# Optimization experiments

Hardware: AMD Instinct MI355X
Metric: run time of the kernel (lower is better)

## Reference

```python
import jax, jax.numpy as jnp
import numpy as np

N_NODES = 50000
N_EDGES = 1_600_000
IN_CH = 128
HID = 128


def setup_inputs() -> dict:
    key = jax.random.key(0)
    ks = jax.random.split(key, 8)
    x = jax.random.normal(ks[0], (N_NODES, IN_CH), dtype=jnp.float32)
    edge_index = jax.random.randint(ks[1], (2, N_EDGES), 0, N_NODES, dtype=jnp.int64)
    def glorot(k, shape):
        fan_in, fan_out = shape
        s = jnp.sqrt(6.0 / (fan_in + fan_out))
        return jax.random.uniform(k, shape, jnp.float32, -s, s)
    return {
        "x": x,
        "edge_index": edge_index,
        "W1": glorot(ks[2], (IN_CH, HID)), "b1": jnp.zeros((HID,), jnp.float32),
        "W2": glorot(ks[3], (HID, HID)), "b2": jnp.zeros((HID,), jnp.float32),
        "W_age": glorot(ks[4], (HID, 3)), "b_age": jnp.zeros((3,), jnp.float32),
        "W_sex": glorot(ks[5], (HID, 2)), "b_sex": jnp.zeros((2,), jnp.float32),
        "W_eth": glorot(ks[6], (HID, 3)), "b_eth": jnp.zeros((3,), jnp.float32),
    }


def _prep_graph(edge_index, n_nodes):
    # PyG GCNConv default: add self-loops, symmetric normalization.
    loops = jnp.arange(n_nodes, dtype=edge_index.dtype)
    src = jnp.concatenate([edge_index[0], loops])
    dst = jnp.concatenate([edge_index[1], loops])
    deg = jax.ops.segment_sum(jnp.ones_like(dst, jnp.float32), dst, num_segments=n_nodes)
    dinv = jnp.where(deg > 0, jax.lax.rsqrt(deg), 0.0)
    norm = dinv[src] * dinv[dst]  # [E+N]
    return src, dst, norm


def _gcn_conv(x, W, b, src, dst, norm, n_nodes):
    h = x @ W                              # [N, out] linear transform first
    msg = h[src] * norm[:, None]           # gather + normalize
    out = jax.ops.segment_sum(msg, dst, num_segments=n_nodes)  # scatter-add
    return out + b


def reference(x, edge_index, W1, b1, W2, b2, W_age, b_age, W_sex, b_sex, W_eth, b_eth):
    n = x.shape[0]
    src, dst, norm = _prep_graph(edge_index, n)
    h = jax.nn.relu(_gcn_conv(x, W1, b1, src, dst, norm, n))
    h = jax.nn.relu(_gcn_conv(h, W2, b2, src, dst, norm, n))
    age = _gcn_conv(h, W_age, b_age, src, dst, norm, n)
    sex = _gcn_conv(h, W_sex, b_sex, src, dst, norm, n)
    eth = _gcn_conv(h, W_eth, b_eth, src, dst, norm, n)
    return age, sex, eth
```

## Files before the change

### kernel.cpp

```cpp
#include <hip/hip_runtime.h>
#include <hip/hip_fp16.h>


#define NBUK_MAX 512

__global__ __launch_bounds__(256) void k_bhist(const int* __restrict__ dst, int E, int nbuk,
                                               int* __restrict__ bcount) {
    __shared__ int h[NBUK_MAX];
    int tid = threadIdx.x;
    for (int i = tid; i < nbuk; i += 256) h[i] = 0;
    __syncthreads();
    int s0 = blockIdx.x * 4096;
#pragma unroll
    for (int i = 0; i < 16; i++) {
        int e = s0 + i * 256 + tid;
        if (e < E) atomicAdd(&h[dst[e] >> 7], 1);
    }
    __syncthreads();
    for (int i = tid; i < nbuk; i += 256)
        if (h[i]) atomicAdd(&bcount[i], h[i]);
}

__global__ __launch_bounds__(512) void k_bscan(const int* __restrict__ bcount, int nb,
                                               int* __restrict__ bbase, int* __restrict__ bcur) {
    __shared__ int s[512];
    int tid = threadIdx.x;
    int v = (tid < nb) ? bcount[tid] : 0;
    s[tid] = v;
    __syncthreads();
    for (int off = 1; off < 512; off <<= 1) {
        int t = (tid >= off) ? s[tid - off] : 0;
        __syncthreads();
        s[tid] += t;
        __syncthreads();
    }
    if (tid < nb) {
        int excl = s[tid] - v;
        bbase[tid] = excl;
        bcur[tid] = excl;
        if (tid == nb - 1) bbase[nb] = s[tid];
    }
}

__global__ __launch_bounds__(256) void k_passA(const int* __restrict__ src,
                                               const int* __restrict__ dst, int E, int nbuk,
                                               int* __restrict__ bcur,
                                               unsigned* __restrict__ bbuf) {
    __shared__ int h[NBUK_MAX];
    __shared__ int base[NBUK_MAX];
    __shared__ int lcur[NBUK_MAX];
    int tid = threadIdx.x;
    for (int i = tid; i < nbuk; i += 256) h[i] = 0;
    __syncthreads();
    int s0 = blockIdx.x * 4096;
#pragma unroll
    for (int i = 0; i < 16; i++) {
        int e = s0 + i * 256 + tid;
        if (e < E) atomicAdd(&h[dst[e] >> 7], 1);
    }
    __syncthreads();
    for (int i = tid; i < nbuk; i += 256) {
        int c = h[i];
        base[i] = c ? atomicAdd(&bcur[i], c) : 0;
        lcur[i] = 0;
    }
    __syncthreads();
#pragma unroll
    for (int i = 0; i < 16; i++) {
        int e = s0 + i * 256 + tid;
        if (e < E) {
            int d = dst[e];
            int b = d >> 7;
            int idx = atomicAdd(&lcur[b], 1);
            bbuf[base[b] + idx] = ((unsigned)d << 16) | (unsigned)src[e];
        }
    }
}

__global__ __launch_bounds__(256) void k_passB(const unsigned* __restrict__ bbuf,
                                               const int* __restrict__ bbase, int N,
                                               int* __restrict__ row_ptr,
                                               float* __restrict__ dinv,
                                               unsigned short* __restrict__ sorted) {
    __shared__ int h[128], sc[128], lc[128];
    int b = blockIdx.x, tid = threadIdx.x;
    int node0 = b << 7;
    int ncnt = min(128, N - node0);
    int s = bbase[b], e = bbase[b + 1];
    if (tid < 128) h[tid] = 0;
    __syncthreads();
    for (int i = s + tid; i < e; i += 256) atomicAdd(&h[(bbuf[i] >> 16) & 127], 1);
    __syncthreads();
    if (tid < 128) sc[tid] = h[tid];
    __syncthreads();
    for (int off = 1; off < 128; off <<= 1) {
        int t = 0;
        if (tid < 128 && tid >= off) t = sc[tid - off];
        __syncthreads();
        if (tid < 128) sc[tid] += t;
        __syncthreads();
    }
    if (tid < ncnt) {
        int excl = sc[tid] - h[tid];
        row_ptr[node0 + tid] = s + excl;
        dinv[node0 + tid] = rsqrtf((float)(h[tid] + 1));
        lc[tid] = excl;
    }
    if (b == gridDim.x - 1 && tid == 0) row_ptr[N] = e;
    __syncthreads();
    for (int i = s + tid; i < e; i += 256) {
        unsigned p = bbuf[i];
        int nl = (p >> 16) & 127;
        int idx = atomicAdd(&lc[nl], 1);
        sorted[s + idx] = (unsigned short)(p & 0xffffu);
    }
}

__global__ __launch_bounds__(256) void k_gemm_scale_h(const float* __restrict__ in,
                                                      const float* __restrict__ W,
                                                      const float* __restrict__ dinv, int N,
                                                      __half* __restrict__ out) {
    __shared__ float Ws[32][128];
    __shared__ float Xs[32][64];
    int tid = threadIdx.x;
    int row0 = blockIdx.x * 64;
    int tc = tid & 15;
    int tr = tid >> 4;
    float acc[4][8];
#pragma unroll
    for (int i = 0; i < 4; i++)
#pragma unroll
        for (int j = 0; j < 8; j++) acc[i][j] = 0.f;

    for (int k0 = 0; k0 < 128; k0 += 32) {
#pragma unroll
        for (int j = 0; j < 4; j++) {
            int u = tid + j * 256;
            int kk = u >> 5, c4 = u & 31;
            *(float4*)&Ws[kk][c4 * 4] = *(const float4*)&W[(k0 + kk) * 128 + c4 * 4];
        }
#pragma unroll
        for (int j = 0; j < 2; j++) {
            int u = tid + j * 256;
            int r = u >> 3, kq = u & 7;
            int row = row0 + r;
            if (row > N - 1) row = N - 1;
            float4 v = *(const float4*)&in[(size_t)row * 128 + k0 + kq * 4];
            Xs[kq * 4 + 0][r] = v.x;
            Xs[kq * 4 + 1][r] = v.y;
            Xs[kq * 4 + 2][r] = v.z;
            Xs[kq * 4 + 3][r] = v.w;
        }
        __syncthreads();
#pragma unroll 8
        for (int kk = 0; kk < 32; kk++) {
            float4 xv = *(const float4*)&Xs[kk][tr * 4];
            float4 wa = *(const float4*)&Ws[kk][tc * 8];
            float4 wb = *(const float4*)&Ws[kk][tc * 8 + 4];
            float xr[4] = {xv.x, xv.y, xv.z, xv.w};
            float wc[8] = {wa.x, wa.y, wa.z, wa.w, wb.x, wb.y, wb.z, wb.w};
#pragma unroll
            for (int i = 0; i < 4; i++)
#pragma unroll
                for (int j = 0; j < 8; j++) acc[i][j] += xr[i] * wc[j];
        }
        __syncthreads();
    }
#pragma unroll
    for (int i = 0; i < 4; i++) {
        int row = row0 + tr * 4 + i;
        if (row < N) {
            float di = dinv[row];
            union {
                uint4 u;
                __half h[8];
            } pk;
#pragma unroll
            for (int j = 0; j < 8; j++) pk.h[j] = __float2half_rn(di * acc[i][j]);
            *(uint4*)&out[(size_t)row * 128 + tc * 8] = pk.u;
        }
    }
}

__global__ __launch_bounds__(256) void k_agg128h(const __half* __restrict__ hs,
                                                 const int* __restrict__ row_ptr,
                                                 const unsigned short* __restrict__ ss,
                                                 const float* __restrict__ dinv,
                                                 const float* __restrict__ bias, int N,
                                                 int do_relu, float* __restrict__ out) {
    int wid = threadIdx.x >> 6;
    int lane = threadIdx.x & 63;
    int node = blockIdx.x * 4 + wid;
    if (node >= N) return;
    const __half2* hp = (const __half2*)hs;
    float2 acc = __half22float2(hp[(size_t)node * 64 + lane]);
    int s = row_ptr[node], e = row_ptr[node + 1];
    int i = s;
    for (; i + 4 <= e; i += 4) {
        int s0 = ss[i], s1 = ss[i + 1], s2 = ss[i + 2], s3 = ss[i + 3];
        float2 v0 = __half22float2(hp[(size_t)s0 * 64 + lane]);
        float2 v1 = __half22float2(hp[(size_t)s1 * 64 + lane]);
        float2 v2 = __half22float2(hp[(size_t)s2 * 64 + lane]);
        float2 v3 = __half22float2(hp[(size_t)s3 * 64 + lane]);
        acc.x += (v0.x + v1.x) + (v2.x + v3.x);
        acc.y += (v0.y + v1.y) + (v2.y + v3.y);
    }
    for (; i < e; i++) {
        float2 v0 = __half22float2(hp[(size_t)ss[i] * 64 + lane]);
        acc.x += v0.x;
        acc.y += v0.y;
    }
    float di = dinv[node];
    int c = lane * 2;
    float2 b = *(const float2*)&bias[c];
    float ox = di * acc.x + b.x;
    float oy = di * acc.y + b.y;
    if (do_relu) {
        ox = fmaxf(ox, 0.f);
        oy = fmaxf(oy, 0.f);
    }
    *(float2*)&out[(size_t)node * 128 + c] = {ox, oy};
}

__global__ __launch_bounds__(256) void k_headgemm(const float* __restrict__ h,
                                                  const float* __restrict__ Wa,
                                                  const float* __restrict__ Wsx,
                                                  const float* __restrict__ We,
                                                  const float* __restrict__ dinv, int N,
                                                  float* __restrict__ ths) {
    __shared__ float Ws8[128][8];
    int tid = threadIdx.x;
#pragma unroll
    for (int j = 0; j < 4; j++) {
        int u = tid + j * 256;
        int k = u >> 3, c = u & 7;
        float v;
        if (c < 3) v = Wa[k * 3 + c];
        else if (c < 5) v = Wsx[k * 2 + (c - 3)];
        else v = We[k * 3 + (c - 5)];
        Ws8[k][c] = v;
    }
    __syncthreads();
    int node = blockIdx.x * 32 + (tid >> 3);
    int col = tid & 7;
    if (node >= N) return;
    const float* hr = &h[(size_t)node * 128];
    float acc = 0.f;
#pragma unroll 4
    for (int k = 0; k < 128; k += 4) {
        float4 hv = *(const float4*)&hr[k];
        acc += hv.x * Ws8[k][col] + hv.y * Ws8[k + 1][col] + hv.z * Ws8[k + 2][col] +
               hv.w * Ws8[k + 3][col];
    }
    ths[(size_t)node * 8 + col] = dinv[node] * acc;
}

__global__ __launch_bounds__(256) void k_agg8(const float* __restrict__ ths,
                                              const int* __restrict__ row_ptr,
                                              const unsigned short* __restrict__ ss,
                                              const float* __restrict__ dinv,
                                              const float* __restrict__ ba,
                                              const float* __restrict__ bs,
                                              const float* __restrict__ be, int N,
                                              float* __restrict__ outp) {
    int tid = threadIdx.x;
    int node = blockIdx.x * 32 + (tid >> 3);
    int j = tid & 7;
    if (node >= N) return;
    float acc = ths[(size_t)node * 8 + j];
    int s = row_ptr[node], e = row_ptr[node + 1];
    for (int i = s; i < e; i++) {
        int sc = ss[i];
        acc += ths[(size_t)sc * 8 + j];
    }
    float bias = (j < 3) ? ba[j] : ((j < 5) ? bs[j - 3] : be[j - 5]);
    float v = dinv[node] * acc + bias;
    if (j < 3) outp[(size_t)node * 3 + j] = v;
    else if (j < 5) outp[(size_t)N * 3 + (size_t)node * 2 + (j - 3)] = v;
    else outp[(size_t)N * 5 + (size_t)node * 3 + (j - 5)] = v;
}

extern "C" void kernel_launch(void* const* d_in, const int* in_sizes, int n_in,
                              void* d_out, int out_size, void* d_ws, size_t ws_size,
                              hipStream_t stream) {
    const float* x = (const float*)d_in[0];
    const int* edge = (const int*)d_in[1];
    const float* W1 = (const float*)d_in[2];
    const float* b1 = (const float*)d_in[3];
    const float* W2 = (const float*)d_in[4];
    const float* b2 = (const float*)d_in[5];
    const float* Wa = (const float*)d_in[6];
    const float* ba = (const float*)d_in[7];
    const float* Wsx = (const float*)d_in[8];
    const float* bs = (const float*)d_in[9];
    const float* We = (const float*)d_in[10];
    const float* be = (const float*)d_in[11];

    int N = in_sizes[0] / 128;
    int E = in_sizes[1] / 2;
    const int* srcp = edge;
    const int* dstp = edge + E;
    int nbuk = (N + 127) >> 7;

    char* ws = (char*)d_ws;
    size_t off = 0;
    auto alloc = [&](size_t bytes) -> char* {
        char* p = ws + off;
        off += (bytes + 255) & ~(size_t)255;
        return p;
    };
    int* bcount = (int*)alloc((size_t)(nbuk + 1) * 4);
    int* bbase = (int*)alloc((size_t)(nbuk + 1) * 4);
    int* bcur = (int*)alloc((size_t)(nbuk + 1) * 4);
    int* row_ptr = (int*)alloc((size_t)(N + 1) * 4);
    float* dinv = (float*)alloc((size_t)N * 4);
    unsigned* bbuf = (unsigned*)alloc((size_t)E * 4);
    unsigned short* sorted = (unsigned short*)alloc((size_t)E * 2);
    __half* bufH = (__half*)alloc((size_t)N * 128 * 2);
    float* bufF = (float*)alloc((size_t)N * 128 * 4);
    float* ths = (float*)alloc((size_t)N * 8 * 4);

    int nbT = (E + 4095) / 4096;

    hipMemsetAsync(bcount, 0, (size_t)(nbuk + 1) * 4, stream);
    k_bhist<<<nbT, 256, 0, stream>>>(dstp, E, nbuk, bcount);
    k_bscan<<<1, 512, 0, stream>>>(bcount, nbuk, bbase, bcur);
    k_passA<<<nbT, 256, 0, stream>>>(srcp, dstp, E, nbuk, bcur, bbuf);
    k_passB<<<nbuk, 256, 0, stream>>>(bbuf, bbase, N, row_ptr, dinv, sorted);

    int gb = (N + 63) / 64;
    k_gemm_scale_h<<<gb, 256, 0, stream>>>(x, W1, dinv, N, bufH);
    k_agg128h<<<(N + 3) / 4, 256, 0, stream>>>(bufH, row_ptr, sorted, dinv, b1, N, 1, bufF);
    k_gemm_scale_h<<<gb, 256, 0, stream>>>(bufF, W2, dinv, N, bufH);
    k_agg128h<<<(N + 3) / 4, 256, 0, stream>>>(bufH, row_ptr, sorted, dinv, b2, N, 1, bufF);
    k_headgemm<<<(N + 31) / 32, 256, 0, stream>>>(bufF, Wa, Wsx, We, dinv, N, ths);
    k_agg8<<<(N + 31) / 32, 256, 0, stream>>>(ths, row_ptr, sorted, dinv, ba, bs, be, N,
                                              (float*)d_out);
}
```

Baseline: 274.5 us.

## Split feature table into 32-channel slabs and aggregate per slab for cache locality

The GEMM output is now stored as four column slabs of 32 half channels each, laid out contiguously per slab. Aggregation runs as four passes, one per slab, with each wave splitting its lanes into four edge groups that are reduced by shuffles. The aim is for each pass's gathered working set to fit in L2, cutting the cost of random gathers. In exchange, the index array is read four times, there are extra kernel launches, and each gather is a smaller 64-byte segment.

```diff
diff --git a/kernel.cpp b/kernel.cpp
--- a/kernel.cpp
+++ b/kernel.cpp
@@ -177,49 +177,61 @@
             } pk;
 #pragma unroll
             for (int j = 0; j < 8; j++) pk.h[j] = __float2half_rn(di * acc[i][j]);
-            *(uint4*)&out[(size_t)row * 128 + tc * 8] = pk.u;
-        }
-    }
-}
-
-__global__ __launch_bounds__(256) void k_agg128h(const __half* __restrict__ hs,
-                                                 const int* __restrict__ row_ptr,
-                                                 const unsigned short* __restrict__ ss,
-                                                 const float* __restrict__ dinv,
-                                                 const float* __restrict__ bias, int N,
-                                                 int do_relu, float* __restrict__ out) {
+            *(uint4*)&out[((size_t)(tc >> 2) * N + row) * 32 + (tc & 3) * 8] = pk.u;
+        }
+    }
+}
+
+__global__ __launch_bounds__(256) void k_agg32(const __half* __restrict__ hs,
+                                               const int* __restrict__ row_ptr,
+                                               const unsigned short* __restrict__ ss,
+                                               const float* __restrict__ dinv,
+                                               const float* __restrict__ bias, int N,
+                                               int c0, int do_relu,
+                                               float* __restrict__ out) {
     int wid = threadIdx.x >> 6;
     int lane = threadIdx.x & 63;
     int node = blockIdx.x * 4 + wid;
     if (node >= N) return;
+    int g = lane >> 4;
+    int cl = lane & 15;
     const __half2* hp = (const __half2*)hs;
-    float2 acc = __half22float2(hp[(size_t)node * 64 + lane]);
+    float2 acc = {0.f, 0.f};
+    {
+        float2 sv = __half22float2(hp[(size_t)node * 16 + cl]);
+        if (g == 0) acc = sv;
+    }
     int s = row_ptr[node], e = row_ptr[node + 1];
-    int i = s;
-    for (; i + 4 <= e; i += 4) {
-        int s0 = ss[i], s1 = ss[i + 1], s2 = ss[i + 2], s3 = ss[i + 3];
-        float2 v0 = __half22float2(hp[(size_t)s0 * 64 + lane]);
-        float2 v1 = __half22float2(hp[(size_t)s1 * 64 + lane]);
-        float2 v2 = __half22float2(hp[(size_t)s2 * 64 + lane]);
-        float2 v3 = __half22float2(hp[(size_t)s3 * 64 + lane]);
-        acc.x += (v0.x + v1.x) + (v2.x + v3.x);
-        acc.y += (v0.y + v1.y) + (v2.y + v3.y);
-    }
-    for (; i < e; i++) {
-        float2 v0 = __half22float2(hp[(size_t)ss[i] * 64 + lane]);
-        acc.x += v0.x;
-        acc.y += v0.y;
-    }
-    float di = dinv[node];
-    int c = lane * 2;
-    float2 b = *(const float2*)&bias[c];
-    float ox = di * acc.x + b.x;
-    float oy = di * acc.y + b.y;
-    if (do_relu) {
-        ox = fmaxf(ox, 0.f);
-        oy = fmaxf(oy, 0.f);
-    }
-    *(float2*)&out[(size_t)node * 128 + c] = {ox, oy};
+    for (int i = s; i < e; i += 8) {
+        int i0 = i + g, i1 = i + 4 + g;
+        if (i1 < e) {
+            int r0 = ss[i0], r1 = ss[i1];
+            float2 v0 = __half22float2(hp[(size_t)r0 * 16 + cl]);
+            float2 v1 = __half22float2(hp[(size_t)r1 * 16 + cl]);
+            acc.x += v0.x + v1.x;
+            acc.y += v0.y + v1.y;
+        } else if (i0 < e) {
+            int r0 = ss[i0];
+            float2 v0 = __half22float2(hp[(size_t)r0 * 16 + cl]);
+            acc.x += v0.x;
+            acc.y += v0.y;
+        }
+    }
+    acc.x += __shfl_xor(acc.x, 16);
+    acc.y += __shfl_xor(acc.y, 16);
+    acc.x += __shfl_xor(acc.x, 32);
+    acc.y += __shfl_xor(acc.y, 32);
+    if (g == 0) {
+        float di = dinv[node];
+        float2 b = *(const float2*)&bias[c0 + cl * 2];
+        float ox = di * acc.x + b.x;
+        float oy = di * acc.y + b.y;
+        if (do_relu) {
+            ox = fmaxf(ox, 0.f);
+            oy = fmaxf(oy, 0.f);
+        }
+        *(float2*)&out[(size_t)node * 128 + c0 + cl * 2] = {ox, oy};
+    }
 }
 
 __global__ __launch_bounds__(256) void k_headgemm(const float* __restrict__ h,
@@ -329,10 +341,15 @@
     k_passB<<<nbuk, 256, 0, stream>>>(bbuf, bbase, N, row_ptr, dinv, sorted);
 
     int gb = (N + 63) / 64;
+    int ab = (N + 3) / 4;
     k_gemm_scale_h<<<gb, 256, 0, stream>>>(x, W1, dinv, N, bufH);
-    k_agg128h<<<(N + 3) / 4, 256, 0, stream>>>(bufH, row_ptr, sorted, dinv, b1, N, 1, bufF);
+    for (int p = 0; p < 4; p++)
+        k_agg32<<<ab, 256, 0, stream>>>(bufH + (size_t)p * N * 32, row_ptr, sorted, dinv,
+                                        b1, N, p * 32, 1, bufF);
     k_gemm_scale_h<<<gb, 256, 0, stream>>>(bufF, W2, dinv, N, bufH);
-    k_agg128h<<<(N + 3) / 4, 256, 0, stream>>>(bufH, row_ptr, sorted, dinv, b2, N, 1, bufF);
+    for (int p = 0; p < 4; p++)
+        k_agg32<<<ab, 256, 0, stream>>>(bufH + (size_t)p * N * 32, row_ptr, sorted, dinv,
+                                        b2, N, p * 32, 1, bufF);
     k_headgemm<<<(N + 31) / 32, 256, 0, stream>>>(bufF, Wa, Wsx, We, dinv, N, ths);
     k_agg8<<<(N + 31) / 32, 256, 0, stream>>>(ths, row_ptr, sorted, dinv, ba, bs, be, N,
                                               (float*)d_out);
```

After: 391.4 us. +42.6%, slower.

## Slice fp16 features into 16-channel planes and gather per slice

Applied to the files above, without the earlier changes.

The GEMM now writes its half-precision output as eight column slices, each laid out as a contiguous N x 16 plane. Aggregation launches one block per node group per slice, and each wave splits into 8 edge groups that each read a 32-byte row from a slice. Partial sums are combined with cross-lane shuffles. The aim is to shrink each slice's working set so it fits in cache and gather locality improves, at the cost of eight times as many blocks, repeated row_ptr and index reads per slice, and shuffle reductions.

```diff
diff --git a/kernel.cpp b/kernel.cpp
--- a/kernel.cpp
+++ b/kernel.cpp
@@ -177,49 +177,61 @@
             } pk;
 #pragma unroll
             for (int j = 0; j < 8; j++) pk.h[j] = __float2half_rn(di * acc[i][j]);
-            *(uint4*)&out[(size_t)row * 128 + tc * 8] = pk.u;
-        }
-    }
-}
-
-__global__ __launch_bounds__(256) void k_agg128h(const __half* __restrict__ hs,
-                                                 const int* __restrict__ row_ptr,
-                                                 const unsigned short* __restrict__ ss,
-                                                 const float* __restrict__ dinv,
-                                                 const float* __restrict__ bias, int N,
-                                                 int do_relu, float* __restrict__ out) {
+            *(uint4*)&out[((size_t)(tc >> 1) * N + row) * 16 + (tc & 1) * 8] = pk.u;
+        }
+    }
+}
+
+__global__ __launch_bounds__(256) void k_aggs16(const __half* __restrict__ hs,
+                                                const int* __restrict__ row_ptr,
+                                                const unsigned short* __restrict__ ss,
+                                                const float* __restrict__ dinv,
+                                                const float* __restrict__ bias, int N,
+                                                int do_relu, float* __restrict__ out) {
+    int slice = blockIdx.x & 7;
+    int nb = blockIdx.x >> 3;
     int wid = threadIdx.x >> 6;
     int lane = threadIdx.x & 63;
-    int node = blockIdx.x * 4 + wid;
+    int node = nb * 4 + wid;
     if (node >= N) return;
-    const __half2* hp = (const __half2*)hs;
-    float2 acc = __half22float2(hp[(size_t)node * 64 + lane]);
+    int g = lane >> 3;
+    int c = lane & 7;
+    const __half2* hp = (const __half2*)(hs + (size_t)slice * N * 16);
+    float2 acc = {0.f, 0.f};
     int s = row_ptr[node], e = row_ptr[node + 1];
-    int i = s;
-    for (; i + 4 <= e; i += 4) {
-        int s0 = ss[i], s1 = ss[i + 1], s2 = ss[i + 2], s3 = ss[i + 3];
-        float2 v0 = __half22float2(hp[(size_t)s0 * 64 + lane]);
-        float2 v1 = __half22float2(hp[(size_t)s1 * 64 + lane]);
-        float2 v2 = __half22float2(hp[(size_t)s2 * 64 + lane]);
-        float2 v3 = __half22float2(hp[(size_t)s3 * 64 + lane]);
-        acc.x += (v0.x + v1.x) + (v2.x + v3.x);
-        acc.y += (v0.y + v1.y) + (v2.y + v3.y);
-    }
-    for (; i < e; i++) {
-        float2 v0 = __half22float2(hp[(size_t)ss[i] * 64 + lane]);
+    int i = s + g;
+    for (; i + 8 < e; i += 16) {
+        int id0 = ss[i], id1 = ss[i + 8];
+        float2 v0 = __half22float2(hp[(size_t)id0 * 8 + c]);
+        float2 v1 = __half22float2(hp[(size_t)id1 * 8 + c]);
+        acc.x += v0.x + v1.x;
+        acc.y += v0.y + v1.y;
+    }
+    if (i < e) {
+        float2 v0 = __half22float2(hp[(size_t)ss[i] * 8 + c]);
         acc.x += v0.x;
         acc.y += v0.y;
     }
-    float di = dinv[node];
-    int c = lane * 2;
-    float2 b = *(const float2*)&bias[c];
-    float ox = di * acc.x + b.x;
-    float oy = di * acc.y + b.y;
-    if (do_relu) {
-        ox = fmaxf(ox, 0.f);
-        oy = fmaxf(oy, 0.f);
-    }
-    *(float2*)&out[(size_t)node * 128 + c] = {ox, oy};
+    acc.x += __shfl_xor(acc.x, 8);
+    acc.y += __shfl_xor(acc.y, 8);
+    acc.x += __shfl_xor(acc.x, 16);
+    acc.y += __shfl_xor(acc.y, 16);
+    acc.x += __shfl_xor(acc.x, 32);
+    acc.y += __shfl_xor(acc.y, 32);
+    if (g == 0) {
+        float2 sv = __half22float2(hp[(size_t)node * 8 + c]);
+        acc.x += sv.x;
+        acc.y += sv.y;
+        float di = dinv[node];
+        float2 b = *(const float2*)&bias[slice * 16 + c * 2];
+        float ox = di * acc.x + b.x;
+        float oy = di * acc.y + b.y;
+        if (do_relu) {
+            ox = fmaxf(ox, 0.f);
+            oy = fmaxf(oy, 0.f);
+        }
+        *(float2*)&out[(size_t)node * 128 + slice * 16 + c * 2] = {ox, oy};
+    }
 }
 
 __global__ __launch_bounds__(256) void k_headgemm(const float* __restrict__ h,
@@ -329,10 +341,11 @@
     k_passB<<<nbuk, 256, 0, stream>>>(bbuf, bbase, N, row_ptr, dinv, sorted);
 
     int gb = (N + 63) / 64;
+    int agrid = 8 * ((N + 3) / 4);
     k_gemm_scale_h<<<gb, 256, 0, stream>>>(x, W1, dinv, N, bufH);
-    k_agg128h<<<(N + 3) / 4, 256, 0, stream>>>(bufH, row_ptr, sorted, dinv, b1, N, 1, bufF);
+    k_aggs16<<<agrid, 256, 0, stream>>>(bufH, row_ptr, sorted, dinv, b1, N, 1, bufF);
     k_gemm_scale_h<<<gb, 256, 0, stream>>>(bufF, W2, dinv, N, bufH);
-    k_agg128h<<<(N + 3) / 4, 256, 0, stream>>>(bufH, row_ptr, sorted, dinv, b2, N, 1, bufF);
+    k_aggs16<<<agrid, 256, 0, stream>>>(bufH, row_ptr, sorted, dinv, b2, N, 1, bufF);
     k_headgemm<<<(N + 31) / 32, 256, 0, stream>>>(bufF, Wa, Wsx, We, dinv, N, ths);
     k_agg8<<<(N + 31) / 32, 256, 0, stream>>>(ths, row_ptr, sorted, dinv, ba, bs, be, N,
                                               (float*)d_out);
```

Result: slower. 402.4 us (+46.6%).
